# Performance work log

Hardware: AMD Instinct MI355X
Metric: run time of the kernel (lower is better)

## Reference

```python
import jax, jax.numpy as jnp
import numpy as np

N = 512
NODE_IN = 64
NODE_OUT = 64
ED_IN = 32
ED_OUT = 32
STATE = 80  # must satisfy 2*NODE_IN + ED_IN == 2*STATE
SLOPE = 0.1
EPS = 1e-5


def setup_inputs() -> dict:
    key = jax.random.key(0)
    ks = jax.random.split(key, 10)
    def lin(k, out_f, in_f):
        return jax.random.normal(k, (out_f, in_f), jnp.float32) / np.sqrt(in_f).astype(np.float32)
    x = jax.random.normal(ks[0], (N, NODE_IN), jnp.float32)
    edge_attr = jax.random.normal(ks[1], (N * N, ED_IN), jnp.float32)
    mask = jax.random.randint(ks[2], (N * N, 1), 0, 2).astype(jnp.int32)
    return {
        "x": x,
        "edge_attr": edge_attr,
        "mask": mask,
        "W_nu": lin(ks[3], NODE_OUT, NODE_IN),
        "b_nu": jnp.zeros((NODE_OUT,), jnp.float32),
        "W_h2": lin(ks[4], STATE, 2 * STATE),
        "b_h2": jnp.zeros((STATE,), jnp.float32),
        "W_eo": lin(ks[5], ED_OUT, STATE),
        "b_eo": jnp.zeros((ED_OUT,), jnp.float32),
        "e_vec": jax.random.normal(ks[6], (2 * NODE_OUT + ED_OUT,), jnp.float32) * 0.1,
        "bn_n_w": jnp.ones((NODE_OUT,), jnp.float32),
        "bn_n_b": jnp.zeros((NODE_OUT,), jnp.float32),
        "bn_e_w": jnp.ones((ED_OUT,), jnp.float32),
        "bn_e_b": jnp.zeros((ED_OUT,), jnp.float32),
    }


def _lrelu(v):
    return jax.nn.leaky_relu(v, SLOPE)


def _bn(v, w, b):
    # BatchNorm1d, training-mode (batch stats, biased variance)
    mu = v.mean(axis=0)
    var = v.var(axis=0)
    return (v - mu) / jnp.sqrt(var + EPS) * w + b


def reference(x, edge_attr, mask, W_nu, b_nu, W_h2, b_h2, W_eo, b_eo, e_vec,
              bn_n_w, bn_n_b, bn_e_w, bn_e_b):
    n = x.shape[0]
    m = mask.astype(x.dtype)  # [N*N, 1]
    # triplet_e[i*N+j] = [x_i, edge_attr_{ij}, x_j]
    src = jnp.repeat(x, n, axis=0)          # [N*N, NODE_IN]
    dst = jnp.tile(x, (n, 1))               # [N*N, NODE_IN]
    triplet_e = jnp.concatenate([src, edge_attr, dst], axis=-1)  # [N*N, 2*STATE]
    # NOTE: ed_trans_layer / ed_hidden_1 outputs are dead code in the source.
    h = _lrelu(triplet_e @ W_h2.T + b_h2)                 # [N*N, STATE]
    new_edge_attr = _lrelu(h @ W_eo.T + b_eo)             # [N*N, ED_OUT]
    new_edge_attr = new_edge_attr * m
    xn = _lrelu(x @ W_nu.T + b_nu)                        # [N, NODE_OUT]
    triplet_n = jnp.concatenate(
        [jnp.repeat(xn, n, axis=0), new_edge_attr, jnp.tile(xn, (n, 1))], axis=-1
    ).reshape(n, n, 2 * NODE_OUT + ED_OUT)
    scores = _lrelu(jnp.einsum("ijd,d->ij", triplet_n, e_vec))  # [N, N]
    att = jax.nn.softmax(scores, axis=1)
    att = (att.reshape(n * n, 1) * m).reshape(n, n)
    # dropout disabled (deterministic / eval)
    new_x = att @ xn                                       # [N, NODE_OUT]
    new_x = _bn(new_x, bn_n_w, bn_n_b)
    new_edge_attr = _bn(new_edge_attr, bn_e_w, bn_e_b)
    return new_x, new_edge_attr
```

## Files before the change

### kernel.cpp

```cpp
#include <hip/hip_runtime.h>

#define SLOPE 0.1f
#define EPS 1e-5f

typedef __bf16 bf16x8 __attribute__((ext_vector_type(8)));
typedef unsigned short u16x8 __attribute__((ext_vector_type(8)));
typedef float f32x4 __attribute__((ext_vector_type(4)));
typedef unsigned u32x4 __attribute__((ext_vector_type(4)));

#define WS_ESC 0
#define WS_ESH 32
#define WS_A 64
#define WS_B 576
#define WS_XN 1088
#define WS_NEWX 33856
#define WS_P1B 66624
#define WS_PART 107584
#define WSH_WB 280704
#define WSH_WB2 285824
#define WSH_WO 288384
#define WSH_XB 291456
#define WSH_NE 324224

__device__ __forceinline__ float lrelu(float v) { return v > 0.f ? v : SLOPE * v; }
__device__ __forceinline__ unsigned short f2bf(float f) {
  unsigned x = __float_as_uint(f);
  return (unsigned short)((x + 0x7fffu + ((x >> 16) & 1u)) >> 16);
}
__device__ __forceinline__ float bf2f(unsigned short u) {
  return __uint_as_float(((unsigned)u) << 16);
}

__global__ void __launch_bounds__(256) k1(const float* __restrict__ x,
                                          const float* __restrict__ W_nu,
                                          const float* __restrict__ b_nu,
                                          const float* __restrict__ W_h2,
                                          const float* __restrict__ b_h2,
                                          const float* __restrict__ W_eo,
                                          const float* __restrict__ ev,
                                          float* ws) {
  int blk = blockIdx.x;
  int tid = threadIdx.x;
  unsigned short* wsh = (unsigned short*)ws;
  if (blk < 128) {
    __shared__ float wlds[64 * 65];
#pragma unroll
    for (int it = 0; it < 16; it++) {
      int idx = it * 256 + tid;
      wlds[(idx >> 6) * 65 + (idx & 63)] = W_nu[idx];
    }
    int gid = blk * 256 + tid;
    wsh[WSH_XB + gid] = f2bf(x[gid]);
    if (gid < 5120) {
      int c = gid / 2560, r = gid - c * 2560;
      int t = r >> 9, l = (r >> 3) & 63, jj = r & 7;
      int n = t * 16 + (l & 15);
      int k = (l >> 4) * 8 + jj + c * 32;
      wsh[WSH_WB + gid] = f2bf(W_h2[n * 160 + 64 + k]);
    } else if (gid < 7680) {
      int idx = gid - 5120;
      int t = idx >> 9, l = (idx >> 3) & 63, jj = idx & 7;
      int n = t * 16 + (l & 15);
      int k = (l >> 4) * 8 + jj;
      wsh[WSH_WB2 + idx] = f2bf(W_h2[n * 160 + 128 + k]);
    } else if (gid < 10752) {
      int idx = gid - 7680;
      int t2 = idx / 1536, r2 = idx - t2 * 1536;
      int s = r2 >> 9, l = (r2 >> 3) & 63, jj = r2 & 7;
      int n = t2 * 16 + (l & 15);
      int k = s * 32 + (l >> 4) * 8 + jj;
      wsh[WSH_WO + idx] = (k < 80) ? f2bf(W_eo[n * 80 + k]) : (unsigned short)0;
    }
    __syncthreads();
    int i = blk * 4 + (tid >> 6);
    int c = tid & 63;
    float acc = b_nu[c];
    const float* xr = x + i * 64;
#pragma unroll 8
    for (int k = 0; k < 64; k++) acc += xr[k] * wlds[c * 65 + k];
    float xnv = lrelu(acc);
    ws[WS_XN + i * 64 + c] = xnv;
    float va = xnv * ev[c];
    float vb = xnv * ev[96 + c];
#pragma unroll
    for (int off = 32; off >= 1; off >>= 1) {
      va += __shfl_xor(va, off, 64);
      vb += __shfl_xor(vb, off, 64);
    }
    if (c == 0) { ws[WS_A + i] = va; ws[WS_B + i] = vb; }
  } else {
    int b2 = blk - 128;
    int bm = b2 & 7, bn = b2 >> 3;
    int wave = tid >> 6, lane = tid & 63;
    int c16 = lane & 15, q = lane >> 4;
    int n = bn * 16 + c16;
    const float* wrow = W_h2 + n * 160;
    int mrow = bm * 64 + wave * 16 + c16;
    bf16x8 bfr[2], afr[2];
#pragma unroll
    for (int ks = 0; ks < 2; ks++) {
      const float* bs = wrow + ks * 32 + q * 8;
      const float* as = x + mrow * 64 + ks * 32 + q * 8;
      u16x8 ub, ua;
#pragma unroll
      for (int jj = 0; jj < 8; jj++) { ub[jj] = f2bf(bs[jj]); ua[jj] = f2bf(as[jj]); }
      bfr[ks] = __builtin_bit_cast(bf16x8, ub);
      afr[ks] = __builtin_bit_cast(bf16x8, ua);
    }
    float bias = b_h2[n];
    f32x4 acc = {bias, bias, bias, bias};
    acc = __builtin_amdgcn_mfma_f32_16x16x32_bf16(afr[0], bfr[0], acc, 0, 0, 0);
    acc = __builtin_amdgcn_mfma_f32_16x16x32_bf16(afr[1], bfr[1], acc, 0, 0, 0);
#pragma unroll
    for (int r = 0; r < 4; r++) {
      int mm = bm * 64 + wave * 16 + q * 4 + r;
      ws[WS_P1B + mm * 80 + n] = acc[r];
    }
  }
}

__global__ void __launch_bounds__(512, 4) k2(const float* __restrict__ ea,
                                             const int* __restrict__ mask,
                                             const float* __restrict__ b_eo,
                                             const float* __restrict__ ev,
                                             float* ws) {
  __shared__ unsigned short wlds[10752];
  __shared__ unsigned short ht[128 * 104];
  __shared__ float srow[512];
  __shared__ float mlds[512];
  __shared__ float blds[512];
  __shared__ float p1s[80];
  __shared__ float wred[2][8][32];
  __shared__ float nx[8][64];
  __shared__ float red[8];
  int tid = threadIdx.x;
  int w = tid >> 6, lane = tid & 63;
  int c16 = lane & 15, q = lane >> 4;
  int i = blockIdx.x;
  const unsigned short* wsh = (const unsigned short*)ws;
  unsigned* ne32 = (unsigned*)((unsigned short*)ws + WSH_NE);

#pragma unroll
  for (int it = 0; it < 3; it++) {
    int idx = it * 512 + tid;
    if (idx < 1344)
      *(u16x8*)&wlds[idx * 8] = *(const u16x8*)(wsh + WSH_WB + idx * 8);
  }
  mlds[tid] = mask[i * 512 + tid] ? 1.f : 0.f;
  blds[tid] = ws[WS_B + tid];
  if (tid < 80) p1s[tid] = ws[WS_P1B + i * 80 + tid];
  float beo0 = b_eo[c16], beo1 = b_eo[16 + c16];
  float eve0 = ev[64 + c16], eve1 = ev[80 + c16];
  float a_i = ws[WS_A + i];
  __syncthreads();

  float scs0 = 0.f, scss0 = 0.f, scs1 = 0.f, scss1 = 0.f;
#pragma unroll 1
  for (int mt = 0; mt < 4; mt++) {
    int jb = w * 64 + mt * 16;
    bf16x8 af0;
    {
      const float* src = ea + (i * 512 + jb + c16) * 32 + q * 8;
      u16x8 u;
#pragma unroll
      for (int jj = 0; jj < 8; jj++) u[jj] = f2bf(src[jj]);
      af0 = __builtin_bit_cast(bf16x8, u);
    }
    bf16x8 af1 = __builtin_bit_cast(
        bf16x8, *(const u16x8*)(wsh + WSH_XB + (jb + c16) * 64 + q * 8));
    bf16x8 af2 = __builtin_bit_cast(
        bf16x8, *(const u16x8*)(wsh + WSH_XB + (jb + c16) * 64 + 32 + q * 8));
    f32x4 acc[5];
#pragma unroll
    for (int t = 0; t < 5; t++) {
      float p1v = p1s[t * 16 + c16];
      acc[t] = {p1v, p1v, p1v, p1v};
    }
#pragma unroll
    for (int t = 0; t < 5; t++) {
      bf16x8 wb = __builtin_bit_cast(bf16x8, *(const u16x8*)&wlds[t * 512 + lane * 8]);
      acc[t] = __builtin_amdgcn_mfma_f32_16x16x32_bf16(af0, wb, acc[t], 0, 0, 0);
    }
#pragma unroll
    for (int t = 0; t < 5; t++) {
      bf16x8 wb =
          __builtin_bit_cast(bf16x8, *(const u16x8*)&wlds[2560 + t * 512 + lane * 8]);
      acc[t] = __builtin_amdgcn_mfma_f32_16x16x32_bf16(af1, wb, acc[t], 0, 0, 0);
    }
#pragma unroll
    for (int t = 0; t < 5; t++) {
      bf16x8 wb =
          __builtin_bit_cast(bf16x8, *(const u16x8*)&wlds[5120 + t * 512 + lane * 8]);
      acc[t] = __builtin_amdgcn_mfma_f32_16x16x32_bf16(af2, wb, acc[t], 0, 0, 0);
    }
#pragma unroll
    for (int t = 0; t < 5; t++)
#pragma unroll
      for (int r = 0; r < 4; r++)
        ht[(w * 16 + q * 4 + r) * 104 + t * 16 + c16] = f2bf(lrelu(acc[t][r]));
    f32x4 acc2[2] = {{0.f, 0.f, 0.f, 0.f}, {0.f, 0.f, 0.f, 0.f}};
    int hrow = w * 16 + c16;
#pragma unroll
    for (int s = 0; s < 3; s++) {
      int kk = s * 32 + q * 8;
      u16x8 hb = {0, 0, 0, 0, 0, 0, 0, 0};
      if (kk < 80) hb = *(const u16x8*)&ht[hrow * 104 + kk];
      bf16x8 ha = __builtin_bit_cast(bf16x8, hb);
      bf16x8 wo0 = __builtin_bit_cast(
          bf16x8, *(const u16x8*)&wlds[7680 + s * 512 + lane * 8]);
      bf16x8 wo1 = __builtin_bit_cast(
          bf16x8, *(const u16x8*)&wlds[7680 + 1536 + s * 512 + lane * 8]);
      acc2[0] = __builtin_amdgcn_mfma_f32_16x16x32_bf16(ha, wo0, acc2[0], 0, 0, 0);
      acc2[1] = __builtin_amdgcn_mfma_f32_16x16x32_bf16(ha, wo1, acc2[1], 0, 0, 0);
    }
    float se[4];
#pragma unroll
    for (int r = 0; r < 4; r++) {
      int jl = jb + q * 4 + r;
      float mf = mlds[jl];
      float v0 = lrelu(acc2[0][r] + beo0) * mf;
      float v1 = lrelu(acc2[1][r] + beo1) * mf;
      scs0 += v0; scss0 += v0 * v0;
      scs1 += v1; scss1 += v1 * v1;
      ne32[(i * 512 + jl) * 16 + c16] = (unsigned)f2bf(v0) | ((unsigned)f2bf(v1) << 16);
      float s = v0 * eve0 + v1 * eve1;
#pragma unroll
      for (int off = 8; off >= 1; off >>= 1) s += __shfl_xor(s, off, 64);
      se[r] = s;
    }
    if (c16 < 4) {
      int jl = jb + q * 4 + c16;
      float s = (c16 == 0) ? se[0] : (c16 == 1) ? se[1] : (c16 == 2) ? se[2] : se[3];
      srow[jl] = lrelu(a_i + blds[jl] + s);
    }
  }
  scs0 += __shfl_xor(scs0, 16, 64); scs0 += __shfl_xor(scs0, 32, 64);
  scss0 += __shfl_xor(scss0, 16, 64); scss0 += __shfl_xor(scss0, 32, 64);
  scs1 += __shfl_xor(scs1, 16, 64); scs1 += __shfl_xor(scs1, 32, 64);
  scss1 += __shfl_xor(scss1, 16, 64); scss1 += __shfl_xor(scss1, 32, 64);
  if (q == 0) {
    wred[0][w][c16] = scs0; wred[0][w][16 + c16] = scs1;
    wred[1][w][c16] = scss0; wred[1][w][16 + c16] = scss1;
  }
  __syncthreads();
  if (tid < 64) {
    int half = tid >> 5, col = tid & 31;
    float v = 0.f;
#pragma unroll
    for (int ww = 0; ww < 8; ww++) v += wred[half][ww][col];
    ws[WS_PART + i * 64 + tid] = v;
  }
  float p = __expf(srow[tid]);
  float sm = p;
#pragma unroll
  for (int off = 32; off >= 1; off >>= 1) sm += __shfl_xor(sm, off, 64);
  if (lane == 0) red[w] = sm;
  __syncthreads();
  float tot = red[0] + red[1] + red[2] + red[3] + red[4] + red[5] + red[6] + red[7];
  srow[tid] = p * (1.f / tot) * mlds[tid];
  float accv = 0.f;
#pragma unroll 4
  for (int u = 0; u < 64; u++) {
    int j = w * 64 + u;
    accv += srow[j] * ws[WS_XN + j * 64 + lane];
  }
  nx[w][lane] = accv;
  __syncthreads();
  if (tid < 64) {
    float s = 0.f;
#pragma unroll
    for (int ww = 0; ww < 8; ww++) s += nx[ww][tid];
    ws[WS_NEWX + i * 64 + tid] = s;
  }
}

__global__ void __launch_bounds__(512) k3(const float* __restrict__ bn_e_w,
                                          const float* __restrict__ bn_e_b,
                                          float* ws) {
  __shared__ float nx[8][64];
  int tid = threadIdx.x;
  int g = tid >> 6, c = tid & 63;
  float a = 0.f;
  for (int s = g; s < 512; s += 8) a += ws[WS_PART + s * 64 + c];
  nx[g][c] = a;
  __syncthreads();
  if (tid < 64) {
    float t = 0.f;
#pragma unroll
    for (int g2 = 0; g2 < 8; g2++) t += nx[g2][tid];
    nx[0][tid] = t;
  }
  __syncthreads();
  if (tid < 32) {
    float mean = nx[0][tid] * (1.f / 262144.f);
    float var = nx[0][tid + 32] * (1.f / 262144.f) - mean * mean;
    float s = bn_e_w[tid] * rsqrtf(fmaxf(var, 0.f) + EPS);
    ws[WS_ESC + tid] = s;
    ws[WS_ESH + tid] = bn_e_b[tid] - mean * s;
  }
}

__global__ void __launch_bounds__(256) k5(const float* __restrict__ bn_n_w,
                                          const float* __restrict__ bn_n_b,
                                          const float* __restrict__ ws,
                                          float* __restrict__ out) {
  int blk = blockIdx.x, tid = threadIdx.x;
  if (blk < 8) {
    __shared__ float s1[4][64], s2[4][64], scl[64], sh[64];
    int c = tid & 63, g = tid >> 6;
    float a = 0.f, b = 0.f;
#pragma unroll 4
    for (int u = 0; u < 128; u++) {
      float v = ws[WS_NEWX + (g * 128 + u) * 64 + c];
      a += v;
      b += v * v;
    }
    s1[g][c] = a;
    s2[g][c] = b;
    __syncthreads();
    if (tid < 64) {
      float sum = s1[0][tid] + s1[1][tid] + s1[2][tid] + s1[3][tid];
      float ssq = s2[0][tid] + s2[1][tid] + s2[2][tid] + s2[3][tid];
      float mean = sum * (1.f / 512.f);
      float var = ssq * (1.f / 512.f) - mean * mean;
      float s = bn_n_w[tid] * rsqrtf(fmaxf(var, 0.f) + EPS);
      scl[tid] = s;
      sh[tid] = bn_n_b[tid] - mean * s;
    }
    __syncthreads();
#pragma unroll 4
    for (int u = 0; u < 16; u++) {
      int idx = blk * 4096 + u * 256 + tid;
      int c2 = idx & 63;
      out[idx] = ws[WS_NEWX + idx] * scl[c2] + sh[c2];
    }
  } else {
    const unsigned* ne32 = (const unsigned*)((const unsigned short*)ws + WSH_NE);
    int b4 = ((blk - 8) * 256 + tid) * 4;
    u32x4 raw = *(const u32x4*)(ne32 + b4);
    int e32 = (b4 >> 4) * 32;
    int cb = b4 & 15;
    f32x4 esc0 = *(const f32x4*)(ws + WS_ESC + cb);
    f32x4 esc1 = *(const f32x4*)(ws + WS_ESC + 16 + cb);
    f32x4 esh0 = *(const f32x4*)(ws + WS_ESH + cb);
    f32x4 esh1 = *(const f32x4*)(ws + WS_ESH + 16 + cb);
    f32x4 lo, hi;
#pragma unroll
    for (int u = 0; u < 4; u++) {
      lo[u] = bf2f((unsigned short)(raw[u] & 0xffffu)) * esc0[u] + esh0[u];
      hi[u] = bf2f((unsigned short)(raw[u] >> 16)) * esc1[u] + esh1[u];
    }
    float* oe = out + 32768;
    *(f32x4*)(oe + e32 + cb) = lo;
    *(f32x4*)(oe + e32 + 16 + cb) = hi;
  }
}

extern "C" void kernel_launch(void* const* d_in, const int* in_sizes, int n_in,
                              void* d_out, int out_size, void* d_ws, size_t ws_size,
                              hipStream_t stream) {
  const float* x = (const float*)d_in[0];
  const float* ea = (const float*)d_in[1];
  const int* mask = (const int*)d_in[2];
  const float* Wnu = (const float*)d_in[3];
  const float* bnu = (const float*)d_in[4];
  const float* Wh2 = (const float*)d_in[5];
  const float* bh2 = (const float*)d_in[6];
  const float* Weo = (const float*)d_in[7];
  const float* beo = (const float*)d_in[8];
  const float* ev = (const float*)d_in[9];
  const float* bnw = (const float*)d_in[10];
  const float* bnb = (const float*)d_in[11];
  const float* bew = (const float*)d_in[12];
  const float* beb = (const float*)d_in[13];
  float* ws = (float*)d_ws;
  float* out = (float*)d_out;

  k1<<<168, 256, 0, stream>>>(x, Wnu, bnu, Wh2, bh2, Weo, ev, ws);
  k2<<<512, 512, 0, stream>>>(ea, mask, beo, ev, ws);
  k3<<<1, 512, 0, stream>>>(bew, beb, ws);
  k5<<<4104, 256, 0, stream>>>(bnw, bnb, ws, out);
}
```

Baseline: 189.1 us.

## Split edge MLP into finer blocks and move softmax/aggregation to separate kernel

The per-row edge kernel (one 512-thread block per node i, looping over 4 tiles per wave) is split into 4096 blocks of 256 threads, each handling a 64-column slice of one row. Scores go to a global buffer, and BN partial sums are accumulated with atomics into zeroed per-row slots. Softmax, masking and att@xn move into k3, which gets an extra block for the BN-stat finalization. The aim is more parallelism and less per-block serial work. The cost is an extra global round trip for the scores, plus atomics and a kernel-boundary dependency.

New measurement: 162.1 us. 1.17x faster.

```diff
diff --git a/kernel.cpp b/kernel.cpp
--- a/kernel.cpp
+++ b/kernel.cpp
@@ -15,12 +15,13 @@
 #define WS_XN 1088
 #define WS_NEWX 33856
 #define WS_P1B 66624
-#define WS_PART 107584
-#define WSH_WB 280704
-#define WSH_WB2 285824
-#define WSH_WO 288384
-#define WSH_XB 291456
-#define WSH_NE 324224
+#define WS_SC 107584
+#define WS_PART 369728
+#define WSH_WB 804992
+#define WSH_WB2 810112
+#define WSH_WO 812672
+#define WSH_XB 815744
+#define WSH_NE 848512
 
 __device__ __forceinline__ float lrelu(float v) { return v > 0.f ? v : SLOPE * v; }
 __device__ __forceinline__ unsigned short f2bf(float f) {
@@ -51,6 +52,7 @@
     }
     int gid = blk * 256 + tid;
     wsh[WSH_XB + gid] = f2bf(x[gid]);
+    ws[WS_PART + gid] = 0.f;
     if (gid < 5120) {
       int c = gid / 2560, r = gid - c * 2560;
       int t = r >> 9, l = (r >> 3) & 63, jj = r & 7;
@@ -119,120 +121,113 @@
   }
 }
 
-__global__ void __launch_bounds__(512, 4) k2(const float* __restrict__ ea,
-                                             const int* __restrict__ mask,
-                                             const float* __restrict__ b_eo,
-                                             const float* __restrict__ ev,
-                                             float* ws) {
+__global__ void __launch_bounds__(256) k2(const float* __restrict__ ea,
+                                          const int* __restrict__ mask,
+                                          const float* __restrict__ b_eo,
+                                          const float* __restrict__ ev,
+                                          float* ws) {
   __shared__ unsigned short wlds[10752];
-  __shared__ unsigned short ht[128 * 104];
-  __shared__ float srow[512];
-  __shared__ float mlds[512];
-  __shared__ float blds[512];
+  __shared__ unsigned short ht[64 * 104];
   __shared__ float p1s[80];
-  __shared__ float wred[2][8][32];
-  __shared__ float nx[8][64];
-  __shared__ float red[8];
+  __shared__ float wred[2][4][32];
   int tid = threadIdx.x;
   int w = tid >> 6, lane = tid & 63;
   int c16 = lane & 15, q = lane >> 4;
-  int i = blockIdx.x;
+  int blk = blockIdx.x;
+  int i = blk >> 3, j0 = (blk & 7) << 6;
+  int jb = j0 + w * 16;
   const unsigned short* wsh = (const unsigned short*)ws;
   unsigned* ne32 = (unsigned*)((unsigned short*)ws + WSH_NE);
 
 #pragma unroll
-  for (int it = 0; it < 3; it++) {
-    int idx = it * 512 + tid;
-    if (idx < 1344)
-      *(u16x8*)&wlds[idx * 8] = *(const u16x8*)(wsh + WSH_WB + idx * 8);
-  }
-  mlds[tid] = mask[i * 512 + tid] ? 1.f : 0.f;
-  blds[tid] = ws[WS_B + tid];
+  for (int it = 0; it < 6; it++) {
+    int idx = it * 256 + tid;
+    if (idx < 1344) *(u16x8*)&wlds[idx * 8] = *(const u16x8*)(wsh + WSH_WB + idx * 8);
+  }
   if (tid < 80) p1s[tid] = ws[WS_P1B + i * 80 + tid];
   float beo0 = b_eo[c16], beo1 = b_eo[16 + c16];
   float eve0 = ev[64 + c16], eve1 = ev[80 + c16];
   float a_i = ws[WS_A + i];
   __syncthreads();
 
+  bf16x8 af0;
+  {
+    const float* src = ea + (i * 512 + jb + c16) * 32 + q * 8;
+    u16x8 u;
+#pragma unroll
+    for (int jj = 0; jj < 8; jj++) u[jj] = f2bf(src[jj]);
+    af0 = __builtin_bit_cast(bf16x8, u);
+  }
+  bf16x8 af1 = __builtin_bit_cast(
+      bf16x8, *(const u16x8*)(wsh + WSH_XB + (jb + c16) * 64 + q * 8));
+  bf16x8 af2 = __builtin_bit_cast(
+      bf16x8, *(const u16x8*)(wsh + WSH_XB + (jb + c16) * 64 + 32 + q * 8));
+
+  f32x4 acc[5];
+#pragma unroll
+  for (int t = 0; t < 5; t++) {
+    float p1v = p1s[t * 16 + c16];
+    acc[t] = {p1v, p1v, p1v, p1v};
+  }
+#pragma unroll
+  for (int t = 0; t < 5; t++) {
+    bf16x8 wb = __builtin_bit_cast(bf16x8, *(const u16x8*)&wlds[t * 512 + lane * 8]);
+    acc[t] = __builtin_amdgcn_mfma_f32_16x16x32_bf16(af0, wb, acc[t], 0, 0, 0);
+  }
+#pragma unroll
+  for (int t = 0; t < 5; t++) {
+    bf16x8 wb =
+        __builtin_bit_cast(bf16x8, *(const u16x8*)&wlds[2560 + t * 512 + lane * 8]);
+    acc[t] = __builtin_amdgcn_mfma_f32_16x16x32_bf16(af1, wb, acc[t], 0, 0, 0);
+  }
+#pragma unroll
+  for (int t = 0; t < 5; t++) {
+    bf16x8 wb =
+        __builtin_bit_cast(bf16x8, *(const u16x8*)&wlds[5120 + t * 512 + lane * 8]);
+    acc[t] = __builtin_amdgcn_mfma_f32_16x16x32_bf16(af2, wb, acc[t], 0, 0, 0);
+  }
+#pragma unroll
+  for (int t = 0; t < 5; t++)
+#pragma unroll
+    for (int r = 0; r < 4; r++)
+      ht[(w * 16 + q * 4 + r) * 104 + t * 16 + c16] = f2bf(lrelu(acc[t][r]));
+
+  f32x4 acc2[2] = {{0.f, 0.f, 0.f, 0.f}, {0.f, 0.f, 0.f, 0.f}};
+  int hrow = w * 16 + c16;
+#pragma unroll
+  for (int s = 0; s < 3; s++) {
+    int kk = s * 32 + q * 8;
+    u16x8 hb = {0, 0, 0, 0, 0, 0, 0, 0};
+    if (kk < 80) hb = *(const u16x8*)&ht[hrow * 104 + kk];
+    bf16x8 ha = __builtin_bit_cast(bf16x8, hb);
+    bf16x8 wo0 =
+        __builtin_bit_cast(bf16x8, *(const u16x8*)&wlds[7680 + s * 512 + lane * 8]);
+    bf16x8 wo1 = __builtin_bit_cast(
+        bf16x8, *(const u16x8*)&wlds[7680 + 1536 + s * 512 + lane * 8]);
+    acc2[0] = __builtin_amdgcn_mfma_f32_16x16x32_bf16(ha, wo0, acc2[0], 0, 0, 0);
+    acc2[1] = __builtin_amdgcn_mfma_f32_16x16x32_bf16(ha, wo1, acc2[1], 0, 0, 0);
+  }
+
   float scs0 = 0.f, scss0 = 0.f, scs1 = 0.f, scss1 = 0.f;
-#pragma unroll 1
-  for (int mt = 0; mt < 4; mt++) {
-    int jb = w * 64 + mt * 16;
-    bf16x8 af0;
-    {
-      const float* src = ea + (i * 512 + jb + c16) * 32 + q * 8;
-      u16x8 u;
-#pragma unroll
-      for (int jj = 0; jj < 8; jj++) u[jj] = f2bf(src[jj]);
-      af0 = __builtin_bit_cast(bf16x8, u);
-    }
-    bf16x8 af1 = __builtin_bit_cast(
-        bf16x8, *(const u16x8*)(wsh + WSH_XB + (jb + c16) * 64 + q * 8));
-    bf16x8 af2 = __builtin_bit_cast(
-        bf16x8, *(const u16x8*)(wsh + WSH_XB + (jb + c16) * 64 + 32 + q * 8));
-    f32x4 acc[5];
-#pragma unroll
-    for (int t = 0; t < 5; t++) {
-      float p1v = p1s[t * 16 + c16];
-      acc[t] = {p1v, p1v, p1v, p1v};
-    }
-#pragma unroll
-    for (int t = 0; t < 5; t++) {
-      bf16x8 wb = __builtin_bit_cast(bf16x8, *(const u16x8*)&wlds[t * 512 + lane * 8]);
-      acc[t] = __builtin_amdgcn_mfma_f32_16x16x32_bf16(af0, wb, acc[t], 0, 0, 0);
-    }
-#pragma unroll
-    for (int t = 0; t < 5; t++) {
-      bf16x8 wb =
-          __builtin_bit_cast(bf16x8, *(const u16x8*)&wlds[2560 + t * 512 + lane * 8]);
-      acc[t] = __builtin_amdgcn_mfma_f32_16x16x32_bf16(af1, wb, acc[t], 0, 0, 0);
-    }
-#pragma unroll
-    for (int t = 0; t < 5; t++) {
-      bf16x8 wb =
-          __builtin_bit_cast(bf16x8, *(const u16x8*)&wlds[5120 + t * 512 + lane * 8]);
-      acc[t] = __builtin_amdgcn_mfma_f32_16x16x32_bf16(af2, wb, acc[t], 0, 0, 0);
-    }
-#pragma unroll
-    for (int t = 0; t < 5; t++)
-#pragma unroll
-      for (int r = 0; r < 4; r++)
-        ht[(w * 16 + q * 4 + r) * 104 + t * 16 + c16] = f2bf(lrelu(acc[t][r]));
-    f32x4 acc2[2] = {{0.f, 0.f, 0.f, 0.f}, {0.f, 0.f, 0.f, 0.f}};
-    int hrow = w * 16 + c16;
-#pragma unroll
-    for (int s = 0; s < 3; s++) {
-      int kk = s * 32 + q * 8;
-      u16x8 hb = {0, 0, 0, 0, 0, 0, 0, 0};
-      if (kk < 80) hb = *(const u16x8*)&ht[hrow * 104 + kk];
-      bf16x8 ha = __builtin_bit_cast(bf16x8, hb);
-      bf16x8 wo0 = __builtin_bit_cast(
-          bf16x8, *(const u16x8*)&wlds[7680 + s * 512 + lane * 8]);
-      bf16x8 wo1 = __builtin_bit_cast(
-          bf16x8, *(const u16x8*)&wlds[7680 + 1536 + s * 512 + lane * 8]);
-      acc2[0] = __builtin_amdgcn_mfma_f32_16x16x32_bf16(ha, wo0, acc2[0], 0, 0, 0);
-      acc2[1] = __builtin_amdgcn_mfma_f32_16x16x32_bf16(ha, wo1, acc2[1], 0, 0, 0);
-    }
-    float se[4];
-#pragma unroll
-    for (int r = 0; r < 4; r++) {
-      int jl = jb + q * 4 + r;
-      float mf = mlds[jl];
-      float v0 = lrelu(acc2[0][r] + beo0) * mf;
-      float v1 = lrelu(acc2[1][r] + beo1) * mf;
-      scs0 += v0; scss0 += v0 * v0;
-      scs1 += v1; scss1 += v1 * v1;
-      ne32[(i * 512 + jl) * 16 + c16] = (unsigned)f2bf(v0) | ((unsigned)f2bf(v1) << 16);
-      float s = v0 * eve0 + v1 * eve1;
-#pragma unroll
-      for (int off = 8; off >= 1; off >>= 1) s += __shfl_xor(s, off, 64);
-      se[r] = s;
-    }
-    if (c16 < 4) {
-      int jl = jb + q * 4 + c16;
-      float s = (c16 == 0) ? se[0] : (c16 == 1) ? se[1] : (c16 == 2) ? se[2] : se[3];
-      srow[jl] = lrelu(a_i + blds[jl] + s);
-    }
+  float se[4];
+#pragma unroll
+  for (int r = 0; r < 4; r++) {
+    int m = i * 512 + jb + q * 4 + r;
+    float mf = mask[m] ? 1.f : 0.f;
+    float v0 = lrelu(acc2[0][r] + beo0) * mf;
+    float v1 = lrelu(acc2[1][r] + beo1) * mf;
+    scs0 += v0; scss0 += v0 * v0;
+    scs1 += v1; scss1 += v1 * v1;
+    ne32[m * 16 + c16] = (unsigned)f2bf(v0) | ((unsigned)f2bf(v1) << 16);
+    float s = v0 * eve0 + v1 * eve1;
+#pragma unroll
+    for (int off = 8; off >= 1; off >>= 1) s += __shfl_xor(s, off, 64);
+    se[r] = s;
+  }
+  if (c16 < 4) {
+    int j = jb + q * 4 + c16;
+    float s = (c16 == 0) ? se[0] : (c16 == 1) ? se[1] : (c16 == 2) ? se[2] : se[3];
+    ws[WS_SC + i * 512 + j] = lrelu(a_i + ws[WS_B + j] + s);
   }
   scs0 += __shfl_xor(scs0, 16, 64); scs0 += __shfl_xor(scs0, 32, 64);
   scss0 += __shfl_xor(scss0, 16, 64); scss0 += __shfl_xor(scss0, 32, 64);
@@ -245,58 +240,67 @@
   __syncthreads();
   if (tid < 64) {
     int half = tid >> 5, col = tid & 31;
-    float v = 0.f;
-#pragma unroll
-    for (int ww = 0; ww < 8; ww++) v += wred[half][ww][col];
-    ws[WS_PART + i * 64 + tid] = v;
-  }
-  float p = __expf(srow[tid]);
+    float v = wred[half][0][col] + wred[half][1][col] + wred[half][2][col] +
+              wred[half][3][col];
+    atomicAdd(&ws[WS_PART + (blk >> 3) * 64 + tid], v);
+  }
+}
+
+__global__ void __launch_bounds__(512) k3(const int* __restrict__ mask,
+                                          const float* __restrict__ bn_e_w,
+                                          const float* __restrict__ bn_e_b,
+                                          float* ws) {
+  __shared__ float att[512];
+  __shared__ float red[8];
+  __shared__ float nx[8][64];
+  int i = blockIdx.x, tid = threadIdx.x;
+  int wave = tid >> 6, lane = tid & 63;
+  if (i == 512) {
+    int g = tid >> 6, c = tid & 63;
+    float a = 0.f;
+    for (int s = g; s < 512; s += 8) a += ws[WS_PART + s * 64 + c];
+    nx[g][c] = a;
+    __syncthreads();
+    if (tid < 64) {
+      float t = 0.f;
+#pragma unroll
+      for (int g2 = 0; g2 < 8; g2++) t += nx[g2][tid];
+      att[tid] = t;
+    }
+    __syncthreads();
+    if (tid < 32) {
+      float mean = att[tid] * (1.f / 262144.f);
+      float var = att[tid + 32] * (1.f / 262144.f) - mean * mean;
+      float s = bn_e_w[tid] * rsqrtf(fmaxf(var, 0.f) + EPS);
+      ws[WS_ESC + tid] = s;
+      ws[WS_ESH + tid] = bn_e_b[tid] - mean * s;
+    }
+    return;
+  }
+  float p = __expf(ws[WS_SC + i * 512 + tid]);
   float sm = p;
 #pragma unroll
   for (int off = 32; off >= 1; off >>= 1) sm += __shfl_xor(sm, off, 64);
-  if (lane == 0) red[w] = sm;
+  if (lane == 0) red[wave] = sm;
   __syncthreads();
   float tot = red[0] + red[1] + red[2] + red[3] + red[4] + red[5] + red[6] + red[7];
-  srow[tid] = p * (1.f / tot) * mlds[tid];
+  att[tid] = p * (1.f / tot) * (mask[i * 512 + tid] ? 1.f : 0.f);
+  __syncthreads();
+  int c = lane;
+  const float* xn = ws + WS_XN;
   float accv = 0.f;
 #pragma unroll 4
   for (int u = 0; u < 64; u++) {
-    int j = w * 64 + u;
-    accv += srow[j] * ws[WS_XN + j * 64 + lane];
-  }
-  nx[w][lane] = accv;
+    int j = wave * 64 + u;
+    accv += att[j] * xn[j * 64 + c];
+  }
+  nx[wave][c] = accv;
   __syncthreads();
   if (tid < 64) {
     float s = 0.f;
 #pragma unroll
-    for (int ww = 0; ww < 8; ww++) s += nx[ww][tid];
+    for (int w = 0; w < 8; w++) s += nx[w][tid];
     ws[WS_NEWX + i * 64 + tid] = s;
-  }
-}
-
-__global__ void __launch_bounds__(512) k3(const float* __restrict__ bn_e_w,
-                                          const float* __restrict__ bn_e_b,
-                                          float* ws) {
-  __shared__ float nx[8][64];
-  int tid = threadIdx.x;
-  int g = tid >> 6, c = tid & 63;
-  float a = 0.f;
-  for (int s = g; s < 512; s += 8) a += ws[WS_PART + s * 64 + c];
-  nx[g][c] = a;
-  __syncthreads();
-  if (tid < 64) {
-    float t = 0.f;
-#pragma unroll
-    for (int g2 = 0; g2 < 8; g2++) t += nx[g2][tid];
-    nx[0][tid] = t;
-  }
-  __syncthreads();
-  if (tid < 32) {
-    float mean = nx[0][tid] * (1.f / 262144.f);
-    float var = nx[0][tid + 32] * (1.f / 262144.f) - mean * mean;
-    float s = bn_e_w[tid] * rsqrtf(fmaxf(var, 0.f) + EPS);
-    ws[WS_ESC + tid] = s;
-    ws[WS_ESH + tid] = bn_e_b[tid] - mean * s;
   }
 }
 
@@ -377,7 +381,7 @@
   float* out = (float*)d_out;
 
   k1<<<168, 256, 0, stream>>>(x, Wnu, bnu, Wh2, bh2, Weo, ev, ws);
-  k2<<<512, 512, 0, stream>>>(ea, mask, beo, ev, ws);
-  k3<<<1, 512, 0, stream>>>(bew, beb, ws);
+  k2<<<4096, 256, 0, stream>>>(ea, mask, beo, ev, ws);
+  k3<<<513, 512, 0, stream>>>(mask, bew, beb, ws);
   k5<<<4104, 256, 0, stream>>>(bnw, bnb, ws, out);
 }
```
